# Performance work log

Measured on AMD Instinct MI355X. Metric: run time of the kernel, lower is better.

## Reference

```python
import jax, jax.numpy as jnp
import numpy as np

N_NODES = 100000
N_EDGES = 1600000
D = 64        # input_dim_nodes == input_dim_edges == output_dim
H = 128       # hidden_dim
LN_EPS = 1e-5


def setup_inputs() -> dict:
    key = jax.random.key(0)
    ks = jax.random.split(key, 9)
    efeat = jax.random.normal(ks[0], (N_EDGES, D), dtype=jnp.float32)
    nfeat = jax.random.normal(ks[1], (N_NODES, D), dtype=jnp.float32)
    dst_idx = jax.random.randint(ks[2], (N_EDGES,), 0, N_NODES, dtype=jnp.int32)
    s1 = 1.0 / np.sqrt(2 * D)
    s2 = 1.0 / np.sqrt(H)
    W1 = jax.random.normal(ks[3], (2 * D, H), dtype=jnp.float32) * s1
    b1 = jnp.zeros((H,), jnp.float32)
    W2 = jax.random.normal(ks[4], (H, D), dtype=jnp.float32) * s2
    b2 = jnp.zeros((D,), jnp.float32)
    gamma = jnp.ones((D,), jnp.float32)
    beta = jnp.zeros((D,), jnp.float32)
    return {"efeat": efeat, "nfeat": nfeat, "dst_idx": dst_idx,
            "W1": W1, "b1": b1, "W2": W2, "b2": b2,
            "gamma": gamma, "beta": beta}


def _layer_norm(x, gamma, beta):
    mu = jnp.mean(x, axis=-1, keepdims=True)
    var = jnp.mean(jnp.square(x - mu), axis=-1, keepdims=True)
    return (x - mu) * jax.lax.rsqrt(var + LN_EPS) * gamma + beta


def reference(efeat, nfeat, dst_idx, W1, b1, W2, b2, gamma, beta):
    # scatter-sum edge features into destination nodes: [E,D] -> [N,D]
    agg = jax.ops.segment_sum(efeat, dst_idx, num_segments=N_NODES)
    # concat(aggregated_edge_feat, node_feat) -> [N, 2D]
    cat_feat = jnp.concatenate([agg, nfeat], axis=-1)
    # MLP: Linear -> SiLU -> Linear -> LayerNorm
    h = jax.nn.silu(cat_feat @ W1 + b1)
    h = h @ W2 + b2
    nfeat_new = _layer_norm(h, gamma, beta) + nfeat
    return (efeat, nfeat_new)
```

## Files before the change

kernel.cpp:

```cpp
#include <hip/hip_runtime.h>
#include <hip/hip_bf16.h>
#include <math.h>

#define N_NODES 100000
#define N_EDGES 1600000
#define D 64
#define H 128
#define LN_EPS 1e-5f

#define NCHUNK ((N_NODES + 1023) / 1024)

__global__ void zero_cnt(int* __restrict__ cnt) {
    int i = blockIdx.x * blockDim.x + threadIdx.x;
    if (i < N_NODES) cnt[i] = 0;
}

__global__ void copy_hist(const float4* __restrict__ ef4,
                          float4* __restrict__ out4,
                          const int* __restrict__ dst,
                          int* __restrict__ cnt) {
    const int total4 = N_EDGES * (D / 4);
    const int stride = gridDim.x * blockDim.x;
    for (int i = blockIdx.x * blockDim.x + threadIdx.x; i < total4; i += stride)
        out4[i] = ef4[i];
    for (int e = blockIdx.x * blockDim.x + threadIdx.x; e < N_EDGES; e += stride)
        atomicAdd(&cnt[dst[e]], 1);
}

__global__ void scan1(const int* __restrict__ cnt,
                      int* __restrict__ starts,
                      int* __restrict__ chunkSum) {
    __shared__ int ps[256];
    const int t = threadIdx.x;
    const int base = blockIdx.x * 1024 + t * 4;
    int v[4];
    #pragma unroll
    for (int r = 0; r < 4; ++r)
        v[r] = (base + r < N_NODES) ? cnt[base + r] : 0;
    int s = v[0] + v[1] + v[2] + v[3];
    ps[t] = s;
    __syncthreads();
    for (int off = 1; off < 256; off <<= 1) {
        int x = (t >= off) ? ps[t - off] : 0;
        __syncthreads();
        ps[t] += x;
        __syncthreads();
    }
    int excl = (t > 0) ? ps[t - 1] : 0;
    int run = excl;
    #pragma unroll
    for (int r = 0; r < 4; ++r) {
        if (base + r < N_NODES) starts[base + r] = run;
        run += v[r];
    }
    if (t == 255) chunkSum[blockIdx.x] = ps[255];
}

__global__ void scan2(const int* __restrict__ chunkSum,
                      int* __restrict__ chunkOff) {
    __shared__ int ps[128];
    const int t = threadIdx.x;
    int own = (t < NCHUNK) ? chunkSum[t] : 0;
    ps[t] = own;
    __syncthreads();
    for (int off = 1; off < 128; off <<= 1) {
        int x = (t >= off) ? ps[t - off] : 0;
        __syncthreads();
        ps[t] += x;
        __syncthreads();
    }
    chunkOff[t] = ps[t] - own;
}

__global__ void scan3(int* __restrict__ starts,
                      const int* __restrict__ chunkOff,
                      int* __restrict__ cursor) {
    const int stride = gridDim.x * blockDim.x;
    for (int i = blockIdx.x * blockDim.x + threadIdx.x; i < N_NODES; i += stride) {
        int s = starts[i] + chunkOff[i >> 10];
        starts[i] = s;
        cursor[i] = s;
    }
}

__global__ void bin_edges(const int* __restrict__ dst,
                          int* __restrict__ cursor,
                          int* __restrict__ eidx) {
    const int stride = gridDim.x * blockDim.x;
    for (int e = blockIdx.x * blockDim.x + threadIdx.x; e < N_EDGES; e += stride) {
        int pos = atomicAdd(&cursor[dst[e]], 1);
        eidx[pos] = e;
    }
}

__device__ __forceinline__ float silu_f(float x) {
    return x / (1.f + __expf(-x));
}

__global__ __launch_bounds__(512, 4)
void fused_mlp(const float* __restrict__ efeat, const float* __restrict__ nfeat,
               const int* __restrict__ starts, const int* __restrict__ cnt,
               const int* __restrict__ eidx,
               const float* __restrict__ W1, const float* __restrict__ b1,
               const float* __restrict__ W2, const float* __restrict__ b2,
               const float* __restrict__ gamma, const float* __restrict__ beta,
               float* __restrict__ out_n) {
    __shared__ float XT[128][132];

    const int tid  = threadIdx.x;
    const int lane = tid & 63;
    const int wave = tid >> 6;
    const int nbase = blockIdx.x * 128;

    const float gl = gamma[lane];
    const float bl = beta[lane];

    float nf[16];
    #pragma unroll 1
    for (int i = 0; i < 16; ++i) {
        const int col = wave * 16 + i;
        const int n = nbase + col;
        float a = 0.f, nv = 0.f;
        if (n < N_NODES) {
            int st  = __builtin_amdgcn_readfirstlane(starts[n]);
            int deg = __builtin_amdgcn_readfirstlane(cnt[n]);
            int eid_l = (lane < deg) ? eidx[st + lane] : 0;
            const int m = deg < 64 ? deg : 64;
            int e = 0;
            for (; e + 8 <= m; e += 8) {
                float v[8];
                #pragma unroll
                for (int j = 0; j < 8; ++j) {
                    int id = __shfl(eid_l, e + j);
                    v[j] = efeat[id * D + lane];
                }
                #pragma unroll
                for (int j = 0; j < 8; ++j) a += v[j];
            }
            for (; e < m; ++e) {
                int id = __shfl(eid_l, e);
                a += efeat[id * D + lane];
            }
            for (; e < deg; ++e)
                a += efeat[eidx[st + e] * D + lane];
            nv = nfeat[(long long)n * D + lane];
        }
        XT[lane][col]      = a;
        XT[64 + lane][col] = nv;
        nf[i] = nv;
    }
    __syncthreads();

    const int nt = tid & 15;
    const int ht = tid >> 4;
    const int j0 = ht * 4;

    float acc0[4][4], acc1[4][4];
    {
        const float4 b4 = *(const float4*)(b1 + j0);
        const float bj[4] = {b4.x, b4.y, b4.z, b4.w};
        #pragma unroll
        for (int i = 0; i < 4; ++i)
            #pragma unroll
            for (int j = 0; j < 4; ++j) { acc0[i][j] = bj[j]; acc1[i][j] = bj[j]; }
    }
    #pragma unroll 4
    for (int k = 0; k < 2 * D; ++k) {
        const float4 w4 = *(const float4*)(W1 + k * H + j0);
        const float4 xa = *(const float4*)(&XT[k][nt * 4]);
        const float4 xb = *(const float4*)(&XT[k][64 + nt * 4]);
        const float wv[4] = {w4.x, w4.y, w4.z, w4.w};
        const float av[4] = {xa.x, xa.y, xa.z, xa.w};
        const float bv[4] = {xb.x, xb.y, xb.z, xb.w};
        #pragma unroll
        for (int i = 0; i < 4; ++i)
            #pragma unroll
            for (int j = 0; j < 4; ++j) {
                acc0[i][j] = fmaf(av[i], wv[j], acc0[i][j]);
                acc1[i][j] = fmaf(bv[i], wv[j], acc1[i][j]);
            }
    }
    __syncthreads();

    #pragma unroll
    for (int j = 0; j < 4; ++j) {
        *(float4*)(&XT[j0 + j][nt * 4]) =
            make_float4(silu_f(acc0[0][j]), silu_f(acc0[1][j]),
                        silu_f(acc0[2][j]), silu_f(acc0[3][j]));
        *(float4*)(&XT[j0 + j][64 + nt * 4]) =
            make_float4(silu_f(acc1[0][j]), silu_f(acc1[1][j]),
                        silu_f(acc1[2][j]), silu_f(acc1[3][j]));
    }
    __syncthreads();

    const int dt = tid >> 4;
    const int d0 = dt * 2;
    float o0[4][2], o1[4][2];
    {
        const float2 b2v = *(const float2*)(b2 + d0);
        #pragma unroll
        for (int i = 0; i < 4; ++i) {
            o0[i][0] = b2v.x; o0[i][1] = b2v.y;
            o1[i][0] = b2v.x; o1[i][1] = b2v.y;
        }
    }
    #pragma unroll 4
    for (int h = 0; h < H; ++h) {
        const float2 w2v = *(const float2*)(W2 + h * D + d0);
        const float4 sa = *(const float4*)(&XT[h][nt * 4]);
        const float4 sb = *(const float4*)(&XT[h][64 + nt * 4]);
        const float sav[4] = {sa.x, sa.y, sa.z, sa.w};
        const float sbv[4] = {sb.x, sb.y, sb.z, sb.w};
        #pragma unroll
        for (int i = 0; i < 4; ++i) {
            o0[i][0] = fmaf(sav[i], w2v.x, o0[i][0]);
            o0[i][1] = fmaf(sav[i], w2v.y, o0[i][1]);
            o1[i][0] = fmaf(sbv[i], w2v.x, o1[i][0]);
            o1[i][1] = fmaf(sbv[i], w2v.y, o1[i][1]);
        }
    }
    __syncthreads();

    float* O = &XT[0][0];
    #pragma unroll
    for (int i = 0; i < 4; ++i) {
        *(float2*)(O + (nt * 4 + i) * 66 + d0)      = make_float2(o0[i][0], o0[i][1]);
        *(float2*)(O + (64 + nt * 4 + i) * 66 + d0) = make_float2(o1[i][0], o1[i][1]);
    }
    __syncthreads();

    #pragma unroll 1
    for (int i = 0; i < 16; ++i) {
        const int col = wave * 16 + i;
        const int gn = nbase + col;
        float x = O[col * 66 + lane];
        float s = x, q = x * x;
        #pragma unroll
        for (int off = 32; off > 0; off >>= 1) {
            s += __shfl_xor(s, off);
            q += __shfl_xor(q, off);
        }
        const float mu  = s * (1.f / 64.f);
        const float var = q * (1.f / 64.f) - mu * mu;
        const float rs  = rsqrtf(var + LN_EPS);
        if (gn < N_NODES)
            out_n[(long long)gn * D + lane] = (x - mu) * rs * gl + bl + nf[i];
    }
}

extern "C" void kernel_launch(void* const* d_in, const int* in_sizes, int n_in,
                              void* d_out, int out_size, void* d_ws, size_t ws_size,
                              hipStream_t stream) {
    const float* efeat = (const float*)d_in[0];
    const float* nfeat = (const float*)d_in[1];
    const int*   dst   = (const int*)  d_in[2];
    const float* W1    = (const float*)d_in[3];
    const float* b1    = (const float*)d_in[4];
    const float* W2    = (const float*)d_in[5];
    const float* b2    = (const float*)d_in[6];
    const float* gamma = (const float*)d_in[7];
    const float* beta  = (const float*)d_in[8];

    float* out_e = (float*)d_out;
    float* out_n = (float*)d_out + (long long)N_EDGES * D;

    int* W      = (int*)d_ws;
    int* eidx   = W;
    int* cnt    = eidx + N_EDGES;
    int* starts = cnt + N_NODES;
    int* cursor = starts + N_NODES;
    int* chunkSum = cursor + N_NODES;
    int* chunkOff = chunkSum + 128;

    zero_cnt <<<(N_NODES + 255) / 256, 256, 0, stream>>>(cnt);
    copy_hist<<<2048, 256, 0, stream>>>((const float4*)efeat, (float4*)out_e,
                                        dst, cnt);
    scan1    <<<NCHUNK, 256, 0, stream>>>(cnt, starts, chunkSum);
    scan2    <<<1, 128, 0, stream>>>(chunkSum, chunkOff);
    scan3    <<<512, 256, 0, stream>>>(starts, chunkOff, cursor);
    bin_edges<<<1024, 256, 0, stream>>>(dst, cursor, eidx);
    fused_mlp<<<(N_NODES + 127) / 128, 512, 0, stream>>>(
        efeat, nfeat, starts, cnt, eidx, W1, b1, W2, b2, gamma, beta, out_n);
}
```

Measured before the change: 1.139 ms.

## Fuse efeat passthrough copy into gather and use float4 edge loads

The separate 400MB efeat-to-output copy leaves the histogram kernel and moves into the fused MLP gather. Each edge row is read once as float4 and written to out_e while being accumulated. The gather now handles four edge rows per wave step (16 lanes per row), with a cross-group shuffle reduction at the end, and loops over degree in chunks of 64. The aim is to avoid reading efeat twice. The cost is that the output copy now uses scattered writes ordered by edge index, and the grid sizes of hist and bin_edges change.

```diff
diff --git a/kernel.cpp b/kernel.cpp
--- a/kernel.cpp
+++ b/kernel.cpp
@@ -15,14 +15,8 @@
     if (i < N_NODES) cnt[i] = 0;
 }
 
-__global__ void copy_hist(const float4* __restrict__ ef4,
-                          float4* __restrict__ out4,
-                          const int* __restrict__ dst,
-                          int* __restrict__ cnt) {
-    const int total4 = N_EDGES * (D / 4);
+__global__ void hist(const int* __restrict__ dst, int* __restrict__ cnt) {
     const int stride = gridDim.x * blockDim.x;
-    for (int i = blockIdx.x * blockDim.x + threadIdx.x; i < total4; i += stride)
-        out4[i] = ef4[i];
     for (int e = blockIdx.x * blockDim.x + threadIdx.x; e < N_EDGES; e += stride)
         atomicAdd(&cnt[dst[e]], 1);
 }
@@ -46,8 +40,7 @@
         ps[t] += x;
         __syncthreads();
     }
-    int excl = (t > 0) ? ps[t - 1] : 0;
-    int run = excl;
+    int run = (t > 0) ? ps[t - 1] : 0;
     #pragma unroll
     for (int r = 0; r < 4; ++r) {
         if (base + r < N_NODES) starts[base + r] = run;
@@ -98,7 +91,8 @@
 }
 
 __global__ __launch_bounds__(512, 4)
-void fused_mlp(const float* __restrict__ efeat, const float* __restrict__ nfeat,
+void fused_mlp(const float4* __restrict__ ef4, float4* __restrict__ out4,
+               const float* __restrict__ nfeat,
                const int* __restrict__ starts, const int* __restrict__ cnt,
                const int* __restrict__ eidx,
                const float* __restrict__ W1, const float* __restrict__ b1,
@@ -110,6 +104,8 @@
     const int tid  = threadIdx.x;
     const int lane = tid & 63;
     const int wave = tid >> 6;
+    const int rg   = lane >> 4;
+    const int q    = lane & 15;
     const int nbase = blockIdx.x * 128;
 
     const float gl = gamma[lane];
@@ -120,40 +116,49 @@
     for (int i = 0; i < 16; ++i) {
         const int col = wave * 16 + i;
         const int n = nbase + col;
-        float a = 0.f, nv = 0.f;
         if (n < N_NODES) {
-            int st  = __builtin_amdgcn_readfirstlane(starts[n]);
-            int deg = __builtin_amdgcn_readfirstlane(cnt[n]);
-            int eid_l = (lane < deg) ? eidx[st + lane] : 0;
-            const int m = deg < 64 ? deg : 64;
-            int e = 0;
-            for (; e + 8 <= m; e += 8) {
-                float v[8];
-                #pragma unroll
-                for (int j = 0; j < 8; ++j) {
-                    int id = __shfl(eid_l, e + j);
-                    v[j] = efeat[id * D + lane];
+            const int st  = __builtin_amdgcn_readfirstlane(starts[n]);
+            const int deg = __builtin_amdgcn_readfirstlane(cnt[n]);
+            float4 acc = make_float4(0.f, 0.f, 0.f, 0.f);
+            for (int base = 0; base < deg; base += 64) {
+                const int m = min(deg - base, 64);
+                int eid_l = (lane < m) ? eidx[st + base + lane] : 0;
+                for (int c = 0; c < m; c += 4) {
+                    const int row = c + rg;
+                    const int id = __shfl(eid_l, row);
+                    if (row < m) {
+                        float4 v = ef4[id * 16 + q];
+                        out4[id * 16 + q] = v;
+                        acc.x += v.x; acc.y += v.y; acc.z += v.z; acc.w += v.w;
+                    }
                 }
-                #pragma unroll
-                for (int j = 0; j < 8; ++j) a += v[j];
-            }
-            for (; e < m; ++e) {
-                int id = __shfl(eid_l, e);
-                a += efeat[id * D + lane];
-            }
-            for (; e < deg; ++e)
-                a += efeat[eidx[st + e] * D + lane];
-            nv = nfeat[(long long)n * D + lane];
-        }
-        XT[lane][col]      = a;
-        XT[64 + lane][col] = nv;
-        nf[i] = nv;
+            }
+            acc.x += __shfl_xor(acc.x, 16); acc.y += __shfl_xor(acc.y, 16);
+            acc.z += __shfl_xor(acc.z, 16); acc.w += __shfl_xor(acc.w, 16);
+            acc.x += __shfl_xor(acc.x, 32); acc.y += __shfl_xor(acc.y, 32);
+            acc.z += __shfl_xor(acc.z, 32); acc.w += __shfl_xor(acc.w, 32);
+            if (lane < 16) {
+                XT[q * 4 + 0][col] = acc.x;
+                XT[q * 4 + 1][col] = acc.y;
+                XT[q * 4 + 2][col] = acc.z;
+                XT[q * 4 + 3][col] = acc.w;
+            }
+            const float nv = nfeat[(long long)n * D + lane];
+            XT[64 + lane][col] = nv;
+            nf[i] = nv;
+        } else {
+            if (lane < 16) {
+                XT[q * 4 + 0][col] = 0.f; XT[q * 4 + 1][col] = 0.f;
+                XT[q * 4 + 2][col] = 0.f; XT[q * 4 + 3][col] = 0.f;
+            }
+            XT[64 + lane][col] = 0.f;
+            nf[i] = 0.f;
+        }
     }
     __syncthreads();
 
     const int nt = tid & 15;
-    const int ht = tid >> 4;
-    const int j0 = ht * 4;
+    const int j0 = (tid >> 4) * 4;
 
     float acc0[4][4], acc1[4][4];
     {
@@ -193,8 +198,7 @@
     }
     __syncthreads();
 
-    const int dt = tid >> 4;
-    const int d0 = dt * 2;
+    const int d0 = (tid >> 4) * 2;
     float o0[4][2], o1[4][2];
     {
         const float2 b2v = *(const float2*)(b2 + d0);
@@ -234,14 +238,14 @@
         const int col = wave * 16 + i;
         const int gn = nbase + col;
         float x = O[col * 66 + lane];
-        float s = x, q = x * x;
+        float s = x, qq = x * x;
         #pragma unroll
         for (int off = 32; off > 0; off >>= 1) {
-            s += __shfl_xor(s, off);
-            q += __shfl_xor(q, off);
+            s  += __shfl_xor(s,  off);
+            qq += __shfl_xor(qq, off);
         }
         const float mu  = s * (1.f / 64.f);
-        const float var = q * (1.f / 64.f) - mu * mu;
+        const float var = qq * (1.f / 64.f) - mu * mu;
         const float rs  = rsqrtf(var + LN_EPS);
         if (gn < N_NODES)
             out_n[(long long)gn * D + lane] = (x - mu) * rs * gl + bl + nf[i];
@@ -264,8 +268,7 @@
     float* out_e = (float*)d_out;
     float* out_n = (float*)d_out + (long long)N_EDGES * D;
 
-    int* W      = (int*)d_ws;
-    int* eidx   = W;
+    int* eidx   = (int*)d_ws;
     int* cnt    = eidx + N_EDGES;
     int* starts = cnt + N_NODES;
     int* cursor = starts + N_NODES;
@@ -273,12 +276,12 @@
     int* chunkOff = chunkSum + 128;
 
     zero_cnt <<<(N_NODES + 255) / 256, 256, 0, stream>>>(cnt);
-    copy_hist<<<2048, 256, 0, stream>>>((const float4*)efeat, (float4*)out_e,
-                                        dst, cnt);
+    hist     <<<1024, 256, 0, stream>>>(dst, cnt);
     scan1    <<<NCHUNK, 256, 0, stream>>>(cnt, starts, chunkSum);
     scan2    <<<1, 128, 0, stream>>>(chunkSum, chunkOff);
     scan3    <<<512, 256, 0, stream>>>(starts, chunkOff, cursor);
-    bin_edges<<<1024, 256, 0, stream>>>(dst, cursor, eidx);
+    bin_edges<<<2048, 256, 0, stream>>>(dst, cursor, eidx);
     fused_mlp<<<(N_NODES + 127) / 128, 512, 0, stream>>>(
-        efeat, nfeat, starts, cnt, eidx, W1, b1, W2, b2, gamma, beta, out_n);
-}
+        (const float4*)efeat, (float4*)out_e, nfeat,
+        starts, cnt, eidx, W1, b1, W2, b2, gamma, beta, out_n);
+}
```

Result: faster. 1.100 ms (-3.4%).
